# Kernel optimization log

Hardware: AMD Instinct MI355X
Metric: run time of the kernel (lower is better)

## Reference

```python
import jax, jax.numpy as jnp
import numpy as np

N = 100000      # num_nodes
E = 1600000     # num_edges (avg degree 16)
IN = 128        # in_feats
OUT = 64        # out_feats
D = 4           # num_divisions


def setup_inputs() -> dict:
    key = jax.random.key(0)
    ks = jax.random.split(key, 6)
    feature = jax.random.normal(ks[0], (N, IN), dtype=jnp.float32)
    # per-division linear weights, stored as [D, out, in] (torch Linear layout)
    W = jax.random.normal(ks[1], (D, OUT, IN), dtype=jnp.float32) * (1.0 / np.sqrt(IN))
    norm = jax.random.uniform(ks[2], (N, 1), dtype=jnp.float32)
    src = jax.random.randint(ks[3], (E,), 0, N)
    dst = jax.random.randint(ks[4], (E,), 0, N)
    edge_div = jax.random.randint(ks[5], (E,), 0, D)
    return {"feature": feature, "W": W, "norm": norm,
            "src": src, "dst": dst, "edge_div": edge_div}


def reference(feature, W, norm, src, dst, edge_div):
    # Per-division linear transform + per-node norm scaling: [D, N, OUT]
    t = jnp.einsum('ni,doi->dno', feature, W) * norm
    # Gather the source-node features for each edge from its division's transform
    msgs = t[edge_div, src]                      # [E, OUT]
    # Scatter-sum to (dst, division) slots in one segment_sum pass
    seg = dst * D + edge_div                     # [E]
    agg = jax.ops.segment_sum(msgs, seg, num_segments=N * D)  # [N*D, OUT]
    # Row order is node-major, division-minor -> reshape == torch.cat over divisions
    h = agg.reshape(N, D * OUT) * norm           # final norm scale
    return jax.nn.relu(h)
```

## Files before the change

kernel.cpp:

```cpp
#include <hip/hip_runtime.h>


#define IN_F   128
#define OUTC   256
#define EPC    4096
#define NBMAX  512
#define STGF   5120

typedef __bf16 bf16x8 __attribute__((ext_vector_type(8)));
typedef float  f32x4  __attribute__((ext_vector_type(4)));

__device__ inline float bf16_to_f32(unsigned short h) {
    return __uint_as_float(((unsigned int)h) << 16);
}

__global__ __launch_bounds__(256) void wsplit_kernel(
    const float* __restrict__ W, __bf16* __restrict__ Whi, __bf16* __restrict__ Wlo)
{
    const int idx = blockIdx.x * 256 + threadIdx.x;
    const float v = W[idx];
    const __bf16 h = (__bf16)v;
    Whi[idx] = h;
    Wlo[idx] = (__bf16)(v - (float)h);
}

__device__ inline void split_bf16x8(const float4 q0, const float4 q1,
                                    bf16x8& h, bf16x8& l)
{
    float av[8] = {q0.x, q0.y, q0.z, q0.w, q1.x, q1.y, q1.z, q1.w};
    #pragma unroll
    for (int i = 0; i < 8; ++i) {
        const __bf16 hb = (__bf16)av[i];
        h[i] = hb;
        l[i] = (__bf16)(av[i] - (float)hb);
    }
}

__global__ __launch_bounds__(256) void gemm_mfma_kernel(
    const float* __restrict__ feat, const __bf16* __restrict__ Whi,
    const __bf16* __restrict__ Wlo, const float* __restrict__ norm,
    __bf16* __restrict__ t, int nNodes)
{
    const int tid  = threadIdx.x;
    const int wave = (blockIdx.x << 2) + (tid >> 6);
    const int lane = tid & 63;
    const int r    = lane & 15;
    const int g    = lane >> 4;
    const int row0 = wave * 32;
    if (row0 >= nNodes) return;

    f32x4 acc[2][16];
    const f32x4 zero = {0.f, 0.f, 0.f, 0.f};
    #pragma unroll
    for (int h = 0; h < 2; ++h)
        #pragma unroll
        for (int c = 0; c < 16; ++c)
            acc[h][c] = zero;

    const int ra0 = row0 + r;
    const int ra1 = row0 + 16 + r;
    const float* pa0 = feat + (size_t)(ra0 < nNodes ? ra0 : 0) * IN_F;
    const float* pa1 = feat + (size_t)(ra1 < nNodes ? ra1 : 0) * IN_F;
    const __bf16* bhp = Whi + r * IN_F;
    const __bf16* blp = Wlo + r * IN_F;

    #pragma unroll
    for (int s = 0; s < 4; ++s) {
        const int koff = s * 32 + g * 8;
        bf16x8 a0h, a0l, a1h, a1l;
        split_bf16x8(*(const float4*)(pa0 + koff), *(const float4*)(pa0 + koff + 4),
                     a0h, a0l);
        split_bf16x8(*(const float4*)(pa1 + koff), *(const float4*)(pa1 + koff + 4),
                     a1h, a1l);
        #pragma unroll
        for (int c = 0; c < 16; ++c) {
            const bf16x8 bh = *(const bf16x8*)(bhp + c * 16 * IN_F + koff);
            const bf16x8 bl = *(const bf16x8*)(blp + c * 16 * IN_F + koff);
            acc[0][c] = __builtin_amdgcn_mfma_f32_16x16x32_bf16(a0h, bh, acc[0][c], 0, 0, 0);
            acc[0][c] = __builtin_amdgcn_mfma_f32_16x16x32_bf16(a0l, bh, acc[0][c], 0, 0, 0);
            acc[0][c] = __builtin_amdgcn_mfma_f32_16x16x32_bf16(a0h, bl, acc[0][c], 0, 0, 0);
            acc[1][c] = __builtin_amdgcn_mfma_f32_16x16x32_bf16(a1h, bh, acc[1][c], 0, 0, 0);
            acc[1][c] = __builtin_amdgcn_mfma_f32_16x16x32_bf16(a1l, bh, acc[1][c], 0, 0, 0);
            acc[1][c] = __builtin_amdgcn_mfma_f32_16x16x32_bf16(a1h, bl, acc[1][c], 0, 0, 0);
        }
    }

    float nv[2][4];
    #pragma unroll
    for (int h = 0; h < 2; ++h)
        #pragma unroll
        for (int j = 0; j < 4; ++j) {
            const int grow = row0 + h * 16 + g * 4 + j;
            nv[h][j] = (grow < nNodes) ? norm[grow] : 0.f;
        }

    #pragma unroll
    for (int h = 0; h < 2; ++h)
        #pragma unroll
        for (int j = 0; j < 4; ++j) {
            const int grow = row0 + h * 16 + g * 4 + j;
            if (grow >= nNodes) continue;
            __bf16* po = t + (size_t)grow * OUTC + r;
            #pragma unroll
            for (int c = 0; c < 16; ++c)
                po[c * 16] = (__bf16)(acc[h][c][j] * nv[h][j]);
        }
}

__global__ __launch_bounds__(256) void bucket_hist_kernel(
    const int* __restrict__ dst, int* __restrict__ bcnt, int nEdges, int nBuck)
{
    __shared__ int h[NBMAX];
    const int tid = threadIdx.x;
    for (int b = tid; b < nBuck; b += 256) h[b] = 0;
    __syncthreads();
    const int e0 = blockIdx.x * EPC;
    const int cnt = min(EPC, nEdges - e0);
    for (int i = tid; i < cnt; i += 256)
        atomicAdd(&h[((unsigned)dst[e0 + i]) >> 8], 1);
    __syncthreads();
    for (int b = tid; b < nBuck; b += 256)
        if (h[b]) atomicAdd(&bcnt[b], h[b]);
}

__global__ __launch_bounds__(256) void bucket_scan_kernel(
    const int* __restrict__ bcnt, int* __restrict__ bbase,
    int* __restrict__ bfront, int nBuck)
{
    __shared__ int wsum[4], woff[4];
    const int tid = threadIdx.x;
    const int i0 = 2 * tid, i1 = 2 * tid + 1;
    const int h0 = (i0 < nBuck) ? bcnt[i0] : 0;
    const int h1 = (i1 < nBuck) ? bcnt[i1] : 0;
    const int s = h0 + h1;
    int incl = s;
    const int lane = tid & 63;
    #pragma unroll
    for (int off = 1; off < 64; off <<= 1) {
        const int o = __shfl_up(incl, off);
        if (lane >= off) incl += o;
    }
    if (lane == 63) wsum[tid >> 6] = incl;
    __syncthreads();
    if (tid == 0) { int r = 0; for (int i = 0; i < 4; ++i) { woff[i] = r; r += wsum[i]; } }
    __syncthreads();
    const int e = incl - s + woff[tid >> 6];
    if (i0 < nBuck) { bbase[i0] = e;      bfront[i0] = e;      }
    if (i1 < nBuck) { bbase[i1] = e + h0; bfront[i1] = e + h0; }
}

__global__ __launch_bounds__(256) void bucket_place_kernel(
    const int* __restrict__ src, const int* __restrict__ dst,
    const int* __restrict__ ediv, int* __restrict__ bfront,
    uint2* __restrict__ rec, int nEdges, int nBuck)
{
    __shared__ uint2 stg[EPC];
    __shared__ unsigned short stgB[EPC];
    __shared__ int hist[NBMAX], excl[NBMAX], cur[NBMAX], gpos[NBMAX];
    __shared__ int wsum[4], woff[4];

    const int tid = threadIdx.x;
    const int e0 = blockIdx.x * EPC;
    const int cnt = min(EPC, nEdges - e0);

    for (int b = tid; b < nBuck; b += 256) hist[b] = 0;
    __syncthreads();

    for (int i = tid; i < cnt; i += 256)
        atomicAdd(&hist[((unsigned)dst[e0 + i]) >> 8], 1);
    __syncthreads();

    {
        const int i0 = 2 * tid, i1 = 2 * tid + 1;
        const int h0 = (i0 < nBuck) ? hist[i0] : 0;
        const int h1 = (i1 < nBuck) ? hist[i1] : 0;
        const int s = h0 + h1;
        int incl = s;
        const int lane = tid & 63;
        #pragma unroll
        for (int off = 1; off < 64; off <<= 1) {
            const int o = __shfl_up(incl, off);
            if (lane >= off) incl += o;
        }
        if (lane == 63) wsum[tid >> 6] = incl;
        __syncthreads();
        if (tid == 0) { int r = 0; for (int i = 0; i < 4; ++i) { woff[i] = r; r += wsum[i]; } }
        __syncthreads();
        const int e = incl - s + woff[tid >> 6];
        if (i0 < nBuck) { excl[i0] = e;      cur[i0] = e;
                          gpos[i0] = h0 ? atomicAdd(&bfront[i0], h0) : 0; }
        if (i1 < nBuck) { excl[i1] = e + h0; cur[i1] = e + h0;
                          gpos[i1] = h1 ? atomicAdd(&bfront[i1], h1) : 0; }
    }
    __syncthreads();

    for (int i = tid; i < cnt; i += 256) {
        const int e = e0 + i;
        const int d = dst[e];
        const int b = ((unsigned)d) >> 8;
        const int lp = atomicAdd(&cur[b], 1);
        stg[lp]  = make_uint2((unsigned)((src[e] << 2) | ediv[e]), (unsigned)d);
        stgB[lp] = (unsigned short)b;
    }
    __syncthreads();

    for (int s2 = tid; s2 < cnt; s2 += 256) {
        const int b = stgB[s2];
        rec[gpos[b] + (s2 - excl[b])] = stg[s2];
    }
}

__global__ __launch_bounds__(256) void bucket_fine_kernel(
    const uint2* __restrict__ rec, const int* __restrict__ bbase,
    const int* __restrict__ bcnt, int* __restrict__ cursor,
    int* __restrict__ payload, int nNodes)
{
    __shared__ int nhist[256], ncur[256];
    __shared__ int pay[STGF];
    __shared__ int wsum[4], woff[4];

    const int tid = threadIdx.x;
    const int b = blockIdx.x;
    const int base = bbase[b];
    const int cnt = bcnt[b];
    const int node0 = b << 8;

    nhist[tid] = 0;
    __syncthreads();
    for (int i = tid; i < cnt; i += 256)
        atomicAdd(&nhist[rec[base + i].y & 255], 1);
    __syncthreads();

    const int v = nhist[tid];
    int incl = v;
    const int lane = tid & 63;
    #pragma unroll
    for (int off = 1; off < 64; off <<= 1) {
        const int o = __shfl_up(incl, off);
        if (lane >= off) incl += o;
    }
    if (lane == 63) wsum[tid >> 6] = incl;
    __syncthreads();
    if (tid == 0) { int r = 0; for (int i = 0; i < 4; ++i) { woff[i] = r; r += wsum[i]; } }
    __syncthreads();
    incl += woff[tid >> 6];
    ncur[tid] = incl - v;
    if (node0 + tid < nNodes) cursor[node0 + tid] = base + incl;
    __syncthreads();

    if (cnt <= STGF) {
        for (int i = tid; i < cnt; i += 256) {
            const uint2 rr = rec[base + i];
            pay[atomicAdd(&ncur[rr.y & 255], 1)] = (int)rr.x;
        }
        __syncthreads();
        for (int i = tid; i < cnt; i += 256) payload[base + i] = pay[i];
    } else {
        for (int i = tid; i < cnt; i += 256) {
            const uint2 rr = rec[base + i];
            payload[base + atomicAdd(&ncur[rr.y & 255], 1)] = (int)rr.x;
        }
    }
}

__global__ __launch_bounds__(256) void aggregate_kernel(
    const unsigned short* __restrict__ t, const int* __restrict__ cursor,
    const int* __restrict__ payload, const float* __restrict__ norm,
    float* __restrict__ out, int nNodes)
{
    const int wave = (int)((blockIdx.x * 256u + threadIdx.x) >> 6);
    const int lane = threadIdx.x & 63;
    if (wave >= nNodes) return;
    const int e0 = (wave == 0) ? 0 : cursor[wave - 1];
    const int e1 = cursor[wave];

    float acc0 = 0.f, acc1 = 0.f, acc2 = 0.f, acc3 = 0.f;
    int e = e0;
    for (; e + 3 < e1; e += 4) {
        const int p0 = payload[e + 0];
        const int p1 = payload[e + 1];
        const int p2 = payload[e + 2];
        const int p3 = payload[e + 3];
        const float v0 = bf16_to_f32(t[(size_t)(p0 >> 2) * OUTC + (p0 & 3) * 64 + lane]);
        const float v1 = bf16_to_f32(t[(size_t)(p1 >> 2) * OUTC + (p1 & 3) * 64 + lane]);
        const float v2 = bf16_to_f32(t[(size_t)(p2 >> 2) * OUTC + (p2 & 3) * 64 + lane]);
        const float v3 = bf16_to_f32(t[(size_t)(p3 >> 2) * OUTC + (p3 & 3) * 64 + lane]);
        const int d0 = p0 & 3, d1 = p1 & 3, d2 = p2 & 3, d3 = p3 & 3;
        acc0 += (d0 == 0 ? v0 : 0.f) + (d1 == 0 ? v1 : 0.f) + (d2 == 0 ? v2 : 0.f) + (d3 == 0 ? v3 : 0.f);
        acc1 += (d0 == 1 ? v0 : 0.f) + (d1 == 1 ? v1 : 0.f) + (d2 == 1 ? v2 : 0.f) + (d3 == 1 ? v3 : 0.f);
        acc2 += (d0 == 2 ? v0 : 0.f) + (d1 == 2 ? v1 : 0.f) + (d2 == 2 ? v2 : 0.f) + (d3 == 2 ? v3 : 0.f);
        acc3 += (d0 == 3 ? v0 : 0.f) + (d1 == 3 ? v1 : 0.f) + (d2 == 3 ? v2 : 0.f) + (d3 == 3 ? v3 : 0.f);
    }
    for (; e < e1; ++e) {
        const int p0 = payload[e];
        const float v0 = bf16_to_f32(t[(size_t)(p0 >> 2) * OUTC + (p0 & 3) * 64 + lane]);
        const int d0 = p0 & 3;
        acc0 += (d0 == 0 ? v0 : 0.f);
        acc1 += (d0 == 1 ? v0 : 0.f);
        acc2 += (d0 == 2 ? v0 : 0.f);
        acc3 += (d0 == 3 ? v0 : 0.f);
    }

    const float nm = norm[wave];
    float* po = out + (size_t)wave * OUTC;
    po[0 * 64 + lane] = fmaxf(acc0 * nm, 0.f);
    po[1 * 64 + lane] = fmaxf(acc1 * nm, 0.f);
    po[2 * 64 + lane] = fmaxf(acc2 * nm, 0.f);
    po[3 * 64 + lane] = fmaxf(acc3 * nm, 0.f);
}

extern "C" void kernel_launch(void* const* d_in, const int* in_sizes, int n_in,
                              void* d_out, int out_size, void* d_ws, size_t ws_size,
                              hipStream_t stream) {
    const float* feat = (const float*)d_in[0];
    const float* W    = (const float*)d_in[1];
    const float* norm = (const float*)d_in[2];
    const int*   src  = (const int*)d_in[3];
    const int*   dst  = (const int*)d_in[4];
    const int*   ediv = (const int*)d_in[5];
    float* out = (float*)d_out;

    const int nNodes = in_sizes[0] / IN_F;
    const int nEdges = in_sizes[3];
    const int nBuck  = (nNodes + 255) >> 8;
    const int nChunk = (nEdges + EPC - 1) / EPC;

    char* ws = (char*)d_ws;
    const size_t t_bytes      = (size_t)nNodes * OUTC * sizeof(unsigned short);
    const size_t rec_bytes    = (size_t)nEdges * sizeof(uint2);
    const size_t pay_bytes    = (size_t)nEdges * sizeof(int);
    const size_t cursor_bytes = (size_t)nNodes * sizeof(int);
    const size_t wsp_bytes    = (size_t)IN_F * OUTC * sizeof(__bf16);

    __bf16* t      = (__bf16*)ws;
    uint2*  rec    = (uint2*)(ws + t_bytes);
    int*    payload= (int*)(ws + t_bytes + rec_bytes);
    int*    cursor = (int*)(ws + t_bytes + rec_bytes + pay_bytes);
    __bf16* Whi    = (__bf16*)(ws + t_bytes + rec_bytes + pay_bytes + cursor_bytes);
    __bf16* Wlo    = (__bf16*)(ws + t_bytes + rec_bytes + pay_bytes + cursor_bytes + wsp_bytes);
    int*    bcnt   = (int*)(ws + t_bytes + rec_bytes + pay_bytes + cursor_bytes + 2 * wsp_bytes);
    int*    bbase  = bcnt + NBMAX;
    int*    bfront = bcnt + 2 * NBMAX;
    (void)ws_size; (void)out_size; (void)n_in;

    hipMemsetAsync(bcnt, 0, nBuck * sizeof(int), stream);
    wsplit_kernel<<<(IN_F * OUTC) / 256, 256, 0, stream>>>(W, Whi, Wlo);
    bucket_hist_kernel<<<nChunk, 256, 0, stream>>>(dst, bcnt, nEdges, nBuck);
    bucket_scan_kernel<<<1, 256, 0, stream>>>(bcnt, bbase, bfront, nBuck);
    bucket_place_kernel<<<nChunk, 256, 0, stream>>>(src, dst, ediv, bfront, rec,
                                                    nEdges, nBuck);
    bucket_fine_kernel<<<nBuck, 256, 0, stream>>>(rec, bbase, bcnt, cursor, payload,
                                                  nNodes);
    const int gWaves  = (nNodes + 31) / 32;
    const int gBlocks = (gWaves + 3) / 4;
    gemm_mfma_kernel<<<gBlocks, 256, 0, stream>>>(feat, Whi, Wlo, norm, t, nNodes);
    aggregate_kernel<<<(nNodes + 3) / 4, 256, 0, stream>>>((const unsigned short*)t,
                                                           cursor, payload, norm,
                                                           out, nNodes);
}
```

Measured before the change: 371.1 us.

## Keep pre-packed split-bf16 weights register-resident in persistent GEMM waves

Weights are now pre-split into hi/lo bf16 and packed in MFMA fragment order by a new pack kernel. The GEMM becomes a persistent grid in which each wave holds its four output-column fragments in registers and loops over 32-row tiles. This removes the per-wave reload of the whole weight matrix from global memory on every tile. The MFMA operands are swapped so each lane stores four contiguous bf16 values per store instead of scattered scalar stores. In exchange, all four waves of a block re-read and re-split the same feature rows, and the register-resident fragments raise register pressure.

```diff
diff --git a/kernel.cpp b/kernel.cpp
--- a/kernel.cpp
+++ b/kernel.cpp
@@ -6,22 +6,13 @@
 #define EPC    4096
 #define NBMAX  512
 #define STGF   5120
+#define GEMM_GRID 512
 
 typedef __bf16 bf16x8 __attribute__((ext_vector_type(8)));
 typedef float  f32x4  __attribute__((ext_vector_type(4)));
 
 __device__ inline float bf16_to_f32(unsigned short h) {
     return __uint_as_float(((unsigned int)h) << 16);
-}
-
-__global__ __launch_bounds__(256) void wsplit_kernel(
-    const float* __restrict__ W, __bf16* __restrict__ Whi, __bf16* __restrict__ Wlo)
-{
-    const int idx = blockIdx.x * 256 + threadIdx.x;
-    const float v = W[idx];
-    const __bf16 h = (__bf16)v;
-    Whi[idx] = h;
-    Wlo[idx] = (__bf16)(v - (float)h);
 }
 
 __device__ inline void split_bf16x8(const float4 q0, const float4 q1,
@@ -36,75 +27,98 @@
     }
 }
 
-__global__ __launch_bounds__(256) void gemm_mfma_kernel(
-    const float* __restrict__ feat, const __bf16* __restrict__ Whi,
-    const __bf16* __restrict__ Wlo, const float* __restrict__ norm,
-    __bf16* __restrict__ t, int nNodes)
+__global__ __launch_bounds__(256) void wpack_kernel(
+    const float* __restrict__ W, bf16x8* __restrict__ Bpack)
+{
+    const int idx  = blockIdx.x * 256 + threadIdx.x;
+    const int lane = idx & 63;
+    const int c    = (idx >> 6) & 15;
+    const int s    = idx >> 10;
+    const int col  = c * 16 + (lane & 15);
+    const int k0   = s * 32 + (lane >> 4) * 8;
+    const float* p = W + col * IN_F + k0;
+    bf16x8 h, l;
+    #pragma unroll
+    for (int e = 0; e < 8; ++e) {
+        const float v = p[e];
+        const __bf16 hb = (__bf16)v;
+        h[e] = hb;
+        l[e] = (__bf16)(v - (float)hb);
+    }
+    Bpack[idx]        = h;
+    Bpack[4096 + idx] = l;
+}
+
+__global__ __launch_bounds__(256, 2) void gemm_mfma_kernel(
+    const float* __restrict__ feat, const bf16x8* __restrict__ Bpack,
+    const float* __restrict__ norm, __bf16* __restrict__ t,
+    int nNodes, int nTiles)
 {
     const int tid  = threadIdx.x;
-    const int wave = (blockIdx.x << 2) + (tid >> 6);
+    const int wid  = tid >> 6;
     const int lane = tid & 63;
     const int r    = lane & 15;
     const int g    = lane >> 4;
-    const int row0 = wave * 32;
-    if (row0 >= nNodes) return;
-
-    f32x4 acc[2][16];
-    const f32x4 zero = {0.f, 0.f, 0.f, 0.f};
-    #pragma unroll
-    for (int h = 0; h < 2; ++h)
-        #pragma unroll
-        for (int c = 0; c < 16; ++c)
-            acc[h][c] = zero;
-
-    const int ra0 = row0 + r;
-    const int ra1 = row0 + 16 + r;
-    const float* pa0 = feat + (size_t)(ra0 < nNodes ? ra0 : 0) * IN_F;
-    const float* pa1 = feat + (size_t)(ra1 < nNodes ? ra1 : 0) * IN_F;
-    const __bf16* bhp = Whi + r * IN_F;
-    const __bf16* blp = Wlo + r * IN_F;
-
-    #pragma unroll
-    for (int s = 0; s < 4; ++s) {
-        const int koff = s * 32 + g * 8;
-        bf16x8 a0h, a0l, a1h, a1l;
-        split_bf16x8(*(const float4*)(pa0 + koff), *(const float4*)(pa0 + koff + 4),
-                     a0h, a0l);
-        split_bf16x8(*(const float4*)(pa1 + koff), *(const float4*)(pa1 + koff + 4),
-                     a1h, a1l);
-        #pragma unroll
-        for (int c = 0; c < 16; ++c) {
-            const bf16x8 bh = *(const bf16x8*)(bhp + c * 16 * IN_F + koff);
-            const bf16x8 bl = *(const bf16x8*)(blp + c * 16 * IN_F + koff);
-            acc[0][c] = __builtin_amdgcn_mfma_f32_16x16x32_bf16(a0h, bh, acc[0][c], 0, 0, 0);
-            acc[0][c] = __builtin_amdgcn_mfma_f32_16x16x32_bf16(a0l, bh, acc[0][c], 0, 0, 0);
-            acc[0][c] = __builtin_amdgcn_mfma_f32_16x16x32_bf16(a0h, bl, acc[0][c], 0, 0, 0);
-            acc[1][c] = __builtin_amdgcn_mfma_f32_16x16x32_bf16(a1h, bh, acc[1][c], 0, 0, 0);
-            acc[1][c] = __builtin_amdgcn_mfma_f32_16x16x32_bf16(a1l, bh, acc[1][c], 0, 0, 0);
-            acc[1][c] = __builtin_amdgcn_mfma_f32_16x16x32_bf16(a1h, bl, acc[1][c], 0, 0, 0);
-        }
-    }
-
-    float nv[2][4];
-    #pragma unroll
-    for (int h = 0; h < 2; ++h)
-        #pragma unroll
-        for (int j = 0; j < 4; ++j) {
-            const int grow = row0 + h * 16 + g * 4 + j;
-            nv[h][j] = (grow < nNodes) ? norm[grow] : 0.f;
-        }
-
-    #pragma unroll
-    for (int h = 0; h < 2; ++h)
-        #pragma unroll
-        for (int j = 0; j < 4; ++j) {
-            const int grow = row0 + h * 16 + g * 4 + j;
+    const int c0   = wid << 2;
+
+    bf16x8 bfh[4][4], bfl[4][4];
+    #pragma unroll
+    for (int s = 0; s < 4; ++s)
+        #pragma unroll
+        for (int cc = 0; cc < 4; ++cc) {
+            bfh[s][cc] = Bpack[(s * 16 + c0 + cc) * 64 + lane];
+            bfl[s][cc] = Bpack[4096 + (s * 16 + c0 + cc) * 64 + lane];
+        }
+
+    for (int tile = blockIdx.x; tile < nTiles; tile += gridDim.x) {
+        const int row0 = tile * 32;
+        const int ra0 = min(row0 + r, nNodes - 1);
+        const int ra1 = min(row0 + 16 + r, nNodes - 1);
+        const float* pa0 = feat + (size_t)ra0 * IN_F;
+        const float* pa1 = feat + (size_t)ra1 * IN_F;
+
+        f32x4 acc[2][4];
+        #pragma unroll
+        for (int h = 0; h < 2; ++h)
+            #pragma unroll
+            for (int cc = 0; cc < 4; ++cc)
+                acc[h][cc] = (f32x4){0.f, 0.f, 0.f, 0.f};
+
+        #pragma unroll
+        for (int s = 0; s < 4; ++s) {
+            const int koff = s * 32 + g * 8;
+            bf16x8 a0h, a0l, a1h, a1l;
+            split_bf16x8(*(const float4*)(pa0 + koff),
+                         *(const float4*)(pa0 + koff + 4), a0h, a0l);
+            split_bf16x8(*(const float4*)(pa1 + koff),
+                         *(const float4*)(pa1 + koff + 4), a1h, a1l);
+            #pragma unroll
+            for (int cc = 0; cc < 4; ++cc) {
+                acc[0][cc] = __builtin_amdgcn_mfma_f32_16x16x32_bf16(bfh[s][cc], a0h, acc[0][cc], 0, 0, 0);
+                acc[0][cc] = __builtin_amdgcn_mfma_f32_16x16x32_bf16(bfh[s][cc], a0l, acc[0][cc], 0, 0, 0);
+                acc[0][cc] = __builtin_amdgcn_mfma_f32_16x16x32_bf16(bfl[s][cc], a0h, acc[0][cc], 0, 0, 0);
+                acc[1][cc] = __builtin_amdgcn_mfma_f32_16x16x32_bf16(bfh[s][cc], a1h, acc[1][cc], 0, 0, 0);
+                acc[1][cc] = __builtin_amdgcn_mfma_f32_16x16x32_bf16(bfh[s][cc], a1l, acc[1][cc], 0, 0, 0);
+                acc[1][cc] = __builtin_amdgcn_mfma_f32_16x16x32_bf16(bfl[s][cc], a1h, acc[1][cc], 0, 0, 0);
+            }
+        }
+
+        #pragma unroll
+        for (int h = 0; h < 2; ++h) {
+            const int grow = row0 + (h << 4) + r;
             if (grow >= nNodes) continue;
-            __bf16* po = t + (size_t)grow * OUTC + r;
+            const float nm = norm[grow];
+            __bf16* po = t + (size_t)grow * OUTC;
             #pragma unroll
-            for (int c = 0; c < 16; ++c)
-                po[c * 16] = (__bf16)(acc[h][c][j] * nv[h][j]);
-        }
+            for (int cc = 0; cc < 4; ++cc) {
+                union { __bf16 b[4]; uint2 u; } pk;
+                #pragma unroll
+                for (int q = 0; q < 4; ++q)
+                    pk.b[q] = (__bf16)(acc[h][cc][q] * nm);
+                *(uint2*)(po + (c0 + cc) * 16 + (g << 2)) = pk.u;
+            }
+        }
+    }
 }
 
 __global__ __launch_bounds__(256) void bucket_hist_kernel(
@@ -324,36 +338,35 @@
     const int nEdges = in_sizes[3];
     const int nBuck  = (nNodes + 255) >> 8;
     const int nChunk = (nEdges + EPC - 1) / EPC;
+    const int nTiles = (nNodes + 31) / 32;
 
     char* ws = (char*)d_ws;
     const size_t t_bytes      = (size_t)nNodes * OUTC * sizeof(unsigned short);
     const size_t rec_bytes    = (size_t)nEdges * sizeof(uint2);
     const size_t pay_bytes    = (size_t)nEdges * sizeof(int);
     const size_t cursor_bytes = (size_t)nNodes * sizeof(int);
-    const size_t wsp_bytes    = (size_t)IN_F * OUTC * sizeof(__bf16);
+    const size_t bp_bytes     = 8192 * sizeof(bf16x8);
 
     __bf16* t      = (__bf16*)ws;
     uint2*  rec    = (uint2*)(ws + t_bytes);
     int*    payload= (int*)(ws + t_bytes + rec_bytes);
     int*    cursor = (int*)(ws + t_bytes + rec_bytes + pay_bytes);
-    __bf16* Whi    = (__bf16*)(ws + t_bytes + rec_bytes + pay_bytes + cursor_bytes);
-    __bf16* Wlo    = (__bf16*)(ws + t_bytes + rec_bytes + pay_bytes + cursor_bytes + wsp_bytes);
-    int*    bcnt   = (int*)(ws + t_bytes + rec_bytes + pay_bytes + cursor_bytes + 2 * wsp_bytes);
+    bf16x8* Bpack  = (bf16x8*)(ws + t_bytes + rec_bytes + pay_bytes + cursor_bytes);
+    int*    bcnt   = (int*)(ws + t_bytes + rec_bytes + pay_bytes + cursor_bytes + bp_bytes);
     int*    bbase  = bcnt + NBMAX;
     int*    bfront = bcnt + 2 * NBMAX;
     (void)ws_size; (void)out_size; (void)n_in;
 
     hipMemsetAsync(bcnt, 0, nBuck * sizeof(int), stream);
-    wsplit_kernel<<<(IN_F * OUTC) / 256, 256, 0, stream>>>(W, Whi, Wlo);
+    wpack_kernel<<<16, 256, 0, stream>>>(W, Bpack);
     bucket_hist_kernel<<<nChunk, 256, 0, stream>>>(dst, bcnt, nEdges, nBuck);
     bucket_scan_kernel<<<1, 256, 0, stream>>>(bcnt, bbase, bfront, nBuck);
     bucket_place_kernel<<<nChunk, 256, 0, stream>>>(src, dst, ediv, bfront, rec,
                                                     nEdges, nBuck);
     bucket_fine_kernel<<<nBuck, 256, 0, stream>>>(rec, bbase, bcnt, cursor, payload,
                                                   nNodes);
-    const int gWaves  = (nNodes + 31) / 32;
-    const int gBlocks = (gWaves + 3) / 4;
-    gemm_mfma_kernel<<<gBlocks, 256, 0, stream>>>(feat, Whi, Wlo, norm, t, nNodes);
+    gemm_mfma_kernel<<<GEMM_GRID, 256, 0, stream>>>(feat, Bpack, norm, t,
+                                                    nNodes, nTiles);
     aggregate_kernel<<<(nNodes + 3) / 4, 256, 0, stream>>>((const unsigned short*)t,
                                                            cursor, payload, norm,
                                                            out, nNodes);
```

After: 335.8 us. -9.5%, faster.
